# Kernel tuning notes

Hardware: AMD Instinct MI355X
Metric: run time of the kernel (lower is better)

The kernel has to match this reference:

```python
import jax, jax.numpy as jnp
import numpy as np

B, O, I, S = 1024, 256, 256, 20  # batch, out_features, in_features, num_segments


def setup_inputs() -> dict:
    key = jax.random.key(0)
    k1, k2 = jax.random.split(key)
    # x uniform in [-1, 1) so every element falls inside the breakpoint grid
    x = jax.random.uniform(k1, (B, I), dtype=jnp.float32, minval=-1.0, maxval=1.0)
    # breakpoints: linspace(-1, 1, S+1) repeated over (O, I) -- as in nn.Parameter init
    breakpoints = jnp.tile(jnp.linspace(-1.0, 1.0, S + 1, dtype=jnp.float32), (O, I, 1))
    values = jax.random.normal(k2, (O, I, S + 1), dtype=jnp.float32) * 0.1
    return {"x": x, "breakpoints": breakpoints, "values": values}


def _edge(bp, val, xc):
    """Piecewise-linear eval for one (out, in) edge.
    bp, val: [S+1] sorted breakpoints / values; xc: [B] inputs for this in-feature.
    Equivalent to the torch masked loop over segments (mask x in [bp_i, bp_{i+1})),
    but finds the unique segment directly via searchsorted (O(log S) instead of O(S)).
    """
    i = jnp.clip(jnp.searchsorted(bp, xc, side="right") - 1, 0, bp.shape[0] - 2)  # [B]
    lo = bp[i]
    hi = bp[i + 1]
    t = (xc - lo) / (hi - lo + 1e-8)
    interp = val[i] * (1.0 - t) + val[i + 1] * t
    # original mask: contributes only when bp_i <= x < bp_{i+1}; out-of-range -> 0
    return jnp.where((xc >= lo) & (xc < hi), interp, 0.0)


def reference(x, breakpoints, values):
    # vmap over out_features (axis 0 of params), then in_features (axis 1 of params,
    # axis 1 of x -> the matching input column). Result: contrib [O, I, B].
    f = jax.vmap(jax.vmap(_edge, in_axes=(0, 0, 1)), in_axes=(0, 0, None))
    contrib = f(breakpoints, values, x)  # [O, I, B]
    return jnp.sum(contrib, axis=1).T  # [B, O]
```

## Files before the change

### kernel.cpp

```cpp
#include <hip/hip_runtime.h>

#define B_ 1024
#define O_ 256
#define I_ 256
#define S_ 20
#define SP 24
#define K_ (I_ * SP)
#define KSPLIT 8
#define NSTEP 8

typedef unsigned int uint32;
typedef __attribute__((ext_vector_type(8))) short bf16x8;
typedef __attribute__((ext_vector_type(4))) float f32x4;

__device__ inline uint32 f2bf(float f) {
    uint32 u = __float_as_uint(f);
    u = (u + 0x7FFFu + ((u >> 16) & 1u)) >> 16;
    return u & 0xFFFFu;
}

__global__ __launch_bounds__(256) void build_vo(const float* __restrict__ values,
                                                uint32* __restrict__ vo) {
    __shared__ float vstage[256 * 21];
    int t = threadIdx.x;
    const uint4* src4 = (const uint4*)(values + (size_t)blockIdx.x * 256 * 21);
    uint4* st4 = (uint4*)vstage;
#pragma unroll
    for (int j = 0; j < 6; ++j) {
        int p = j * 256 + t;
        if (p < 1344) st4[p] = src4[p];
    }
    __syncthreads();

    const float* v = vstage + t * 21;
    uint32 u[12];
#pragma unroll
    for (int j = 0; j < 12; ++j) {
        int s0 = 2 * j, s1 = 2 * j + 1;
        uint32 lo16 = (s0 <= S_) ? f2bf(v[s0 <= S_ ? s0 : 0]) : 0u;
        uint32 hi16 = (s1 <= S_) ? f2bf(v[s1 <= S_ ? s1 : 0]) : 0u;
        u[j] = lo16 | (hi16 << 16);
    }
    uint4* dst = (uint4*)(vo + ((size_t)blockIdx.x * 256 + t) * 12);
    dst[0] = make_uint4(u[0], u[1], u[2], u[3]);
    dst[1] = make_uint4(u[4], u[5], u[6], u[7]);
    dst[2] = make_uint4(u[8], u[9], u[10], u[11]);
}

__global__ __launch_bounds__(256, 2) void kan_fused(const float* __restrict__ x,
                                                    const float* __restrict__ bp,
                                                    const uint4* __restrict__ vo4,
                                                    ushort* __restrict__ part) {
    __shared__ uint4 Als[2 * 768];
    __shared__ uint4 Bls[2 * 768];

    int L = blockIdx.x;
    int kc = L & 7;
    int rest = L >> 3;
    int mt = rest & 15;
    int nt = rest >> 4;
    int l = threadIdx.x, w = threadIdx.y;
    int t = w * 64 + l;
    int wm = w & 1, wn = w >> 1;
    int lr = l & 15, lg = l >> 4;
    int m0 = mt * 64, n0 = nt * 64;

    float bpr[S_ + 1];
#pragma unroll
    for (int q = 0; q <= S_; ++q) bpr[q] = bp[q];

    int arow = t >> 2, ag = t & 3;
    const float* xp = x + (size_t)(m0 + arow) * I_ + kc * 32 + ag;
    int awo = arow * 12 + 3 * ag;

    int brow = t >> 2, bj = t & 3;
    const uint4* bgp = vo4 + (size_t)(n0 + brow) * (K_ / 8) + kc * 96 + bj;
    int bwo = brow * 12 + bj;

    int fro = lr * 12 + lg;
    int afo0 = (wm * 2 + 0) * 192 + fro;
    int afo1 = (wm * 2 + 1) * 192 + fro;
    int bfo0 = (wn * 2 + 0) * 192 + fro;
    int bfo1 = (wn * 2 + 1) * 192 + fro;

    float xs[NSTEP];
#pragma unroll
    for (int s = 0; s < NSTEP; ++s) xs[s] = xp[s * 4];
    uint4 nb0 = bgp[0], nb1 = bgp[4], nb2 = bgp[8];

    f32x4 acc[2][2] = {};

#define BUILDA(S, Q) do { \
        float xv = xs[S]; \
        int k = -1; \
        float lo = bpr[0], hi = bpr[1]; \
        _Pragma("unroll") \
        for (int q_ = 0; q_ <= S_; ++q_) { \
            bool c = bpr[q_] <= xv; \
            k += c ? 1 : 0; \
            if (q_ >= 1 && q_ <= S_ - 1) { \
                lo = c ? bpr[q_] : lo; \
                hi = c ? bpr[q_ + 1] : hi; \
            } \
        } \
        k = min(max(k, 0), S_ - 1); \
        float tt = (xv - lo) / (hi - lo + 1e-8f); \
        bool inb = (xv >= lo) && (xv < hi); \
        uint32 bw0v = f2bf(inb ? (1.0f - tt) : 0.0f); \
        uint32 bw1v = f2bf(inb ? tt : 0.0f); \
        bool keven = (k & 1) == 0; \
        uint32 wA = keven ? (bw0v | (bw1v << 16)) : (bw0v << 16); \
        uint32 wB = keven ? 0u : bw1v; \
        uint4* ab = Als + (Q) * 768 + awo; \
        uint4 z4 = make_uint4(0u, 0u, 0u, 0u); \
        ab[0] = z4; ab[1] = z4; ab[2] = z4; \
        uint32* abw = (uint32*)ab; \
        int wo = k >> 1; \
        abw[wo] = wA; \
        abw[wo + 1] = wB; \
    } while (0)

#define STOREB(Q) do { \
        uint4* bb = Bls + (Q) * 768 + bwo; \
        bb[0] = nb0; bb[4] = nb1; bb[8] = nb2; \
    } while (0)

#define LOADB(S) do { \
        nb0 = bgp[(S) * 12 + 0]; \
        nb1 = bgp[(S) * 12 + 4]; \
        nb2 = bgp[(S) * 12 + 8]; \
    } while (0)

#define COMPUTE(Q) do { \
        const uint4* ab = Als + (Q) * 768; \
        const uint4* bb = Bls + (Q) * 768; \
        _Pragma("unroll") \
        for (int kk = 0; kk < 3; ++kk) { \
            bf16x8 a0 = *(const bf16x8*)(ab + afo0 + kk * 4); \
            bf16x8 a1 = *(const bf16x8*)(ab + afo1 + kk * 4); \
            bf16x8 b0 = *(const bf16x8*)(bb + bfo0 + kk * 4); \
            bf16x8 b1 = *(const bf16x8*)(bb + bfo1 + kk * 4); \
            acc[0][0] = __builtin_amdgcn_mfma_f32_16x16x32_bf16(a0, b0, acc[0][0], 0, 0, 0); \
            acc[0][1] = __builtin_amdgcn_mfma_f32_16x16x32_bf16(a0, b1, acc[0][1], 0, 0, 0); \
            acc[1][0] = __builtin_amdgcn_mfma_f32_16x16x32_bf16(a1, b0, acc[1][0], 0, 0, 0); \
            acc[1][1] = __builtin_amdgcn_mfma_f32_16x16x32_bf16(a1, b1, acc[1][1], 0, 0, 0); \
        } \
    } while (0)

    BUILDA(0, 0);
    STOREB(0);
    LOADB(1);
    __syncthreads();

#pragma unroll
    for (int s = 0; s < NSTEP; ++s) {
        int q = s & 1, nq = q ^ 1;
        if (s < NSTEP - 1) {
            BUILDA(s + 1, nq);
            STOREB(nq);
            if (s < NSTEP - 2) LOADB(s + 2);
        }
        COMPUTE(q);
        __syncthreads();
    }

#undef BUILDA
#undef STOREB
#undef LOADB
#undef COMPUTE

    ushort* pb = part + ((size_t)kc * B_ * O_)
               + (size_t)(m0 + wm * 32 + lg * 4) * O_ + n0 + wn * 32 + lr;
#pragma unroll
    for (int mi = 0; mi < 2; ++mi)
#pragma unroll
        for (int ni = 0; ni < 2; ++ni)
#pragma unroll
            for (int r = 0; r < 4; ++r)
                pb[(size_t)(mi * 16 + r) * O_ + ni * 16] = (ushort)f2bf(acc[mi][ni][r]);
}

__global__ __launch_bounds__(256) void kan_reduce(const uint4* __restrict__ part4,
                                                  float4* __restrict__ out) {
    int idx = blockIdx.x * 256 + threadIdx.x;
    const int Q = B_ * O_ / 8;
    float s[8] = {0, 0, 0, 0, 0, 0, 0, 0};
#pragma unroll
    for (int c = 0; c < KSPLIT; ++c) {
        uint4 a = part4[(size_t)c * Q + idx];
        s[0] += __uint_as_float(a.x << 16);
        s[1] += __uint_as_float(a.x & 0xFFFF0000u);
        s[2] += __uint_as_float(a.y << 16);
        s[3] += __uint_as_float(a.y & 0xFFFF0000u);
        s[4] += __uint_as_float(a.z << 16);
        s[5] += __uint_as_float(a.z & 0xFFFF0000u);
        s[6] += __uint_as_float(a.w << 16);
        s[7] += __uint_as_float(a.w & 0xFFFF0000u);
    }
    out[idx * 2 + 0] = make_float4(s[0], s[1], s[2], s[3]);
    out[idx * 2 + 1] = make_float4(s[4], s[5], s[6], s[7]);
}

extern "C" void kernel_launch(void* const* d_in, const int* in_sizes, int n_in,
                              void* d_out, int out_size, void* d_ws, size_t ws_size,
                              hipStream_t stream) {
    const float* x      = (const float*)d_in[0];
    const float* bps    = (const float*)d_in[1];
    const float* values = (const float*)d_in[2];
    float* out = (float*)d_out;

    char* ws = (char*)d_ws;
    uint32* vo   = (uint32*)(ws);
    ushort* part = (ushort*)(ws + 3145728);

    build_vo<<<dim3(O_ * I_ / 256), dim3(256), 0, stream>>>(values, vo);
    kan_fused<<<dim3(512), dim3(64, 4), 0, stream>>>(x, bps, (const uint4*)vo, part);
    kan_reduce<<<dim3(B_ * O_ / 8 / 256), dim3(256), 0, stream>>>((const uint4*)part,
                                                                  (float4*)out);
}
```

Baseline: 22.75 us.

## Widen block tile to full N and double the K split

Each block of the fused kernel now covers all 256 output columns and a 16-feature K chunk, using 8 waves instead of 4. The grid is 256 blocks over 16 M tiles and 16 K chunks. The bf16 A tile of segment weights is built once per M tile instead of once per N tile, which removes four-fold redundant breakpoint search and interpolation. In exchange, half the threads idle during A construction and KSPLIT doubles to 16. That doubles the bf16 partial-sum buffer written by the fused kernel and read by the reduce kernel, and the larger partial buffer needs more workspace.

```diff
diff --git a/kernel.cpp b/kernel.cpp
--- a/kernel.cpp
+++ b/kernel.cpp
@@ -6,8 +6,8 @@
 #define S_ 20
 #define SP 24
 #define K_ (I_ * SP)
-#define KSPLIT 8
-#define NSTEP 8
+#define KSPLIT 16
+#define NSTEP 4
 
 typedef unsigned int uint32;
 typedef __attribute__((ext_vector_type(8))) short bf16x8;
@@ -47,103 +47,113 @@
     dst[2] = make_uint4(u[8], u[9], u[10], u[11]);
 }
 
-__global__ __launch_bounds__(256, 2) void kan_fused(const float* __restrict__ x,
+__global__ __launch_bounds__(512, 2) void kan_fused(const float* __restrict__ x,
                                                     const float* __restrict__ bp,
                                                     const uint4* __restrict__ vo4,
                                                     ushort* __restrict__ part) {
     __shared__ uint4 Als[2 * 768];
-    __shared__ uint4 Bls[2 * 768];
+    __shared__ uint4 Bls[2 * 3072];
 
     int L = blockIdx.x;
-    int kc = L & 7;
-    int rest = L >> 3;
-    int mt = rest & 15;
-    int nt = rest >> 4;
+    int kc = ((L & 7) << 1) | ((L >> 3) & 1);
+    int mt = L >> 4;
     int l = threadIdx.x, w = threadIdx.y;
     int t = w * 64 + l;
     int wm = w & 1, wn = w >> 1;
     int lr = l & 15, lg = l >> 4;
-    int m0 = mt * 64, n0 = nt * 64;
+    int m0 = mt * 64;
 
     float bpr[S_ + 1];
 #pragma unroll
     for (int q = 0; q <= S_; ++q) bpr[q] = bp[q];
 
-    int arow = t >> 2, ag = t & 3;
-    const float* xp = x + (size_t)(m0 + arow) * I_ + kc * 32 + ag;
+    int arow = (t >> 2) & 63, ag = t & 3;
+    const float* xp = x + (size_t)(m0 + arow) * I_ + kc * 16 + ag;
     int awo = arow * 12 + 3 * ag;
 
     int brow = t >> 2, bj = t & 3;
-    const uint4* bgp = vo4 + (size_t)(n0 + brow) * (K_ / 8) + kc * 96 + bj;
+    const uint4* bgp  = vo4 + (size_t)brow * (K_ / 8) + kc * 48 + bj;
+    const uint4* bgp2 = bgp + (size_t)128 * (K_ / 8);
     int bwo = brow * 12 + bj;
 
     int fro = lr * 12 + lg;
     int afo0 = (wm * 2 + 0) * 192 + fro;
     int afo1 = (wm * 2 + 1) * 192 + fro;
-    int bfo0 = (wn * 2 + 0) * 192 + fro;
-    int bfo1 = (wn * 2 + 1) * 192 + fro;
+    int bfoB = wn * 4 * 192 + fro;
 
     float xs[NSTEP];
-#pragma unroll
-    for (int s = 0; s < NSTEP; ++s) xs[s] = xp[s * 4];
-    uint4 nb0 = bgp[0], nb1 = bgp[4], nb2 = bgp[8];
-
-    f32x4 acc[2][2] = {};
+    if (t < 256) {
+#pragma unroll
+        for (int s = 0; s < NSTEP; ++s) xs[s] = xp[s * 4];
+    }
+    uint4 nb[6];
+    nb[0] = bgp[0];  nb[1] = bgp[4];  nb[2] = bgp[8];
+    nb[3] = bgp2[0]; nb[4] = bgp2[4]; nb[5] = bgp2[8];
+
+    f32x4 acc[2][4] = {};
 
 #define BUILDA(S, Q) do { \
-        float xv = xs[S]; \
-        int k = -1; \
-        float lo = bpr[0], hi = bpr[1]; \
-        _Pragma("unroll") \
-        for (int q_ = 0; q_ <= S_; ++q_) { \
-            bool c = bpr[q_] <= xv; \
-            k += c ? 1 : 0; \
-            if (q_ >= 1 && q_ <= S_ - 1) { \
-                lo = c ? bpr[q_] : lo; \
-                hi = c ? bpr[q_ + 1] : hi; \
+        if (t < 256) { \
+            float xv = xs[S]; \
+            int k = -1; \
+            float lo = bpr[0], hi = bpr[1]; \
+            _Pragma("unroll") \
+            for (int q_ = 0; q_ <= S_; ++q_) { \
+                bool c = bpr[q_] <= xv; \
+                k += c ? 1 : 0; \
+                if (q_ >= 1 && q_ <= S_ - 1) { \
+                    lo = c ? bpr[q_] : lo; \
+                    hi = c ? bpr[q_ + 1] : hi; \
+                } \
             } \
+            k = min(max(k, 0), S_ - 1); \
+            float tt = (xv - lo) / (hi - lo + 1e-8f); \
+            bool inb = (xv >= lo) && (xv < hi); \
+            uint32 bw0v = f2bf(inb ? (1.0f - tt) : 0.0f); \
+            uint32 bw1v = f2bf(inb ? tt : 0.0f); \
+            bool keven = (k & 1) == 0; \
+            uint32 wA = keven ? (bw0v | (bw1v << 16)) : (bw0v << 16); \
+            uint32 wB = keven ? 0u : bw1v; \
+            uint4* ab = Als + (Q) * 768 + awo; \
+            uint4 z4 = make_uint4(0u, 0u, 0u, 0u); \
+            ab[0] = z4; ab[1] = z4; ab[2] = z4; \
+            uint32* abw = (uint32*)ab; \
+            int wo = k >> 1; \
+            abw[wo] = wA; \
+            abw[wo + 1] = wB; \
         } \
-        k = min(max(k, 0), S_ - 1); \
-        float tt = (xv - lo) / (hi - lo + 1e-8f); \
-        bool inb = (xv >= lo) && (xv < hi); \
-        uint32 bw0v = f2bf(inb ? (1.0f - tt) : 0.0f); \
-        uint32 bw1v = f2bf(inb ? tt : 0.0f); \
-        bool keven = (k & 1) == 0; \
-        uint32 wA = keven ? (bw0v | (bw1v << 16)) : (bw0v << 16); \
-        uint32 wB = keven ? 0u : bw1v; \
-        uint4* ab = Als + (Q) * 768 + awo; \
-        uint4 z4 = make_uint4(0u, 0u, 0u, 0u); \
-        ab[0] = z4; ab[1] = z4; ab[2] = z4; \
-        uint32* abw = (uint32*)ab; \
-        int wo = k >> 1; \
-        abw[wo] = wA; \
-        abw[wo + 1] = wB; \
     } while (0)
 
 #define STOREB(Q) do { \
-        uint4* bb = Bls + (Q) * 768 + bwo; \
-        bb[0] = nb0; bb[4] = nb1; bb[8] = nb2; \
+        uint4* bb = Bls + (Q) * 3072 + bwo; \
+        bb[0] = nb[0]; bb[4] = nb[1]; bb[8] = nb[2]; \
+        bb[1536] = nb[3]; bb[1540] = nb[4]; bb[1544] = nb[5]; \
     } while (0)
 
 #define LOADB(S) do { \
-        nb0 = bgp[(S) * 12 + 0]; \
-        nb1 = bgp[(S) * 12 + 4]; \
-        nb2 = bgp[(S) * 12 + 8]; \
+        nb[0] = bgp[(S) * 12 + 0];  nb[1] = bgp[(S) * 12 + 4];  nb[2] = bgp[(S) * 12 + 8]; \
+        nb[3] = bgp2[(S) * 12 + 0]; nb[4] = bgp2[(S) * 12 + 4]; nb[5] = bgp2[(S) * 12 + 8]; \
     } while (0)
 
 #define COMPUTE(Q) do { \
         const uint4* ab = Als + (Q) * 768; \
-        const uint4* bb = Bls + (Q) * 768; \
+        const uint4* bb = Bls + (Q) * 3072; \
         _Pragma("unroll") \
         for (int kk = 0; kk < 3; ++kk) { \
             bf16x8 a0 = *(const bf16x8*)(ab + afo0 + kk * 4); \
             bf16x8 a1 = *(const bf16x8*)(ab + afo1 + kk * 4); \
-            bf16x8 b0 = *(const bf16x8*)(bb + bfo0 + kk * 4); \
-            bf16x8 b1 = *(const bf16x8*)(bb + bfo1 + kk * 4); \
+            bf16x8 b0 = *(const bf16x8*)(bb + bfoB + 0 * 192 + kk * 4); \
+            bf16x8 b1 = *(const bf16x8*)(bb + bfoB + 1 * 192 + kk * 4); \
+            bf16x8 b2 = *(const bf16x8*)(bb + bfoB + 2 * 192 + kk * 4); \
+            bf16x8 b3 = *(const bf16x8*)(bb + bfoB + 3 * 192 + kk * 4); \
             acc[0][0] = __builtin_amdgcn_mfma_f32_16x16x32_bf16(a0, b0, acc[0][0], 0, 0, 0); \
             acc[0][1] = __builtin_amdgcn_mfma_f32_16x16x32_bf16(a0, b1, acc[0][1], 0, 0, 0); \
+            acc[0][2] = __builtin_amdgcn_mfma_f32_16x16x32_bf16(a0, b2, acc[0][2], 0, 0, 0); \
+            acc[0][3] = __builtin_amdgcn_mfma_f32_16x16x32_bf16(a0, b3, acc[0][3], 0, 0, 0); \
             acc[1][0] = __builtin_amdgcn_mfma_f32_16x16x32_bf16(a1, b0, acc[1][0], 0, 0, 0); \
             acc[1][1] = __builtin_amdgcn_mfma_f32_16x16x32_bf16(a1, b1, acc[1][1], 0, 0, 0); \
+            acc[1][2] = __builtin_amdgcn_mfma_f32_16x16x32_bf16(a1, b2, acc[1][2], 0, 0, 0); \
+            acc[1][3] = __builtin_amdgcn_mfma_f32_16x16x32_bf16(a1, b3, acc[1][3], 0, 0, 0); \
         } \
     } while (0)
 
@@ -170,14 +180,14 @@
 #undef COMPUTE
 
     ushort* pb = part + ((size_t)kc * B_ * O_)
-               + (size_t)(m0 + wm * 32 + lg * 4) * O_ + n0 + wn * 32 + lr;
+               + (size_t)(m0 + wm * 32 + lg * 4) * O_ + wn * 64 + lr;
 #pragma unroll
     for (int mi = 0; mi < 2; ++mi)
 #pragma unroll
-        for (int ni = 0; ni < 2; ++ni)
+        for (int nj = 0; nj < 4; ++nj)
 #pragma unroll
             for (int r = 0; r < 4; ++r)
-                pb[(size_t)(mi * 16 + r) * O_ + ni * 16] = (ushort)f2bf(acc[mi][ni][r]);
+                pb[(size_t)(mi * 16 + r) * O_ + nj * 16] = (ushort)f2bf(acc[mi][nj][r]);
 }
 
 __global__ __launch_bounds__(256) void kan_reduce(const uint4* __restrict__ part4,
@@ -214,7 +224,7 @@
     ushort* part = (ushort*)(ws + 3145728);
 
     build_vo<<<dim3(O_ * I_ / 256), dim3(256), 0, stream>>>(values, vo);
-    kan_fused<<<dim3(512), dim3(64, 4), 0, stream>>>(x, bps, (const uint4*)vo, part);
+    kan_fused<<<dim3(256), dim3(64, 8), 0, stream>>>(x, bps, (const uint4*)vo, part);
     kan_reduce<<<dim3(B_ * O_ / 8 / 256), dim3(256), 0, stream>>>((const uint4*)part,
                                                                   (float4*)out);
 }
```

Measured after the change: 32.00 us. 40.7% more time.
